# Kernel optimization log

Hardware: AMD Instinct MI355X
Metric: run time of the kernel (lower is better)

## Reference

```python
import jax, jax.numpy as jnp
import numpy as np


def setup_inputs() -> dict:
    key = jax.random.key(0)
    ks = jax.random.split(key, 8)
    B, C, H, W = 4, 256, 56, 56
    Cq = C // 8
    s = 0.05  # small init scale for conv weights, like kaiming-ish for 1x1 convs
    return {
        "x": jax.random.normal(ks[0], (B, C, H, W), jnp.float32),
        "Wq": jax.random.normal(ks[1], (Cq, C), jnp.float32) * s,
        "bq": jax.random.normal(ks[2], (Cq,), jnp.float32) * s,
        "Wk": jax.random.normal(ks[3], (Cq, C), jnp.float32) * s,
        "bk": jax.random.normal(ks[4], (Cq,), jnp.float32) * s,
        "Wv": jax.random.normal(ks[5], (C, C), jnp.float32) * s,
        "bv": jax.random.normal(ks[6], (C,), jnp.float32) * s,
        "gamma": jax.random.normal(ks[7], (1,), jnp.float32),
    }


def reference(x, Wq, bq, Wk, bk, Wv, bv, gamma):
    B, C, H, W = x.shape
    N = H * W
    xf = x.reshape(B, C, N)  # flatten spatial

    # 1x1 convs == channel matmuls
    q = jnp.einsum('oc,bcn->bon', Wq, xf) + bq[None, :, None]   # [B,Cq,N]
    k = jnp.einsum('oc,bcn->bon', Wk, xf) + bk[None, :, None]   # [B,Cq,N]
    v = jnp.einsum('oc,bcn->bon', Wv, xf) + bv[None, :, None]   # [B,C,N]

    # lipschitz_norm from weights: u=||Q||_F, v=max row-norm of K^T, w=max row-norm of V^T
    u = jnp.linalg.norm(Wq)
    vn = jnp.max(jnp.linalg.norm(Wk.T, axis=1))
    wn = jnp.max(jnp.linalg.norm(Wv.T, axis=1))
    norm_value = jnp.maximum(u * vn, u * wn)  # maximum(u*v, v*u, u*w)

    # energy[b,i,j] = <q[:,i], k[:,j]>, scaled by custom Lipschitz norm
    energy = jnp.einsum('bci,bcj->bij', q, k) / norm_value      # [B,N,N]
    attention = jax.nn.softmax(energy, axis=-1)

    # out[b,c,i] = sum_j v[b,c,j] * attention[b,i,j]
    out = jnp.einsum('bcj,bij->bci', v, attention).reshape(B, C, H, W)

    # lipschitz_bound: exp(sqrt(3)) * sqrt(N/C) + 2*sqrt(6)
    bound = np.float32(np.exp(np.sqrt(3.0)) * np.sqrt(N / C) + 2.0 * np.sqrt(6.0))
    out = out / bound

    return gamma * out + x
```

## Files before the change

kernel.cpp:

```cpp
#include <hip/hip_runtime.h>

#define N_SP 3136
#define C_CH 256
#define CQ   32
#define NB   4
#define JT   64
#define NJT  49
#define QT   64
#define INV_BOUND 0.04051569f
#define LOG2E 1.44269504f

typedef __attribute__((ext_vector_type(8))) short bf16x8;
typedef __attribute__((ext_vector_type(4))) float f32x4;
typedef __attribute__((ext_vector_type(2))) long long l64x2;
typedef unsigned short u16;
typedef unsigned int   u32;
typedef unsigned char  u8;
typedef long long      l64;

#define MFMA16(a,b,c) __builtin_amdgcn_mfma_f32_16x16x32_bf16(a,b,c,0,0,0)
#define MFMA8(a,b,c)  __builtin_amdgcn_mfma_f32_16x16x32_bf8_fp8(a,b,c,0,0,0)

__device__ __forceinline__ u16 f2b(float f) {
    u32 u = __builtin_bit_cast(u32, f);
    u += 0x7fffu + ((u >> 16) & 1u);
    return (u16)(u >> 16);
}
__device__ __forceinline__ u8 f2fp8(float f) {
    return (u8)(__builtin_amdgcn_cvt_pk_fp8_f32(f, f, 0, false) & 0xff);
}
__device__ __forceinline__ void dma16(const void* g, void* l) {
    __builtin_amdgcn_global_load_lds((const __attribute__((address_space(1))) u32*)g,
                                     (__attribute__((address_space(3))) u32*)l, 16, 0, 0);
}

__global__ __launch_bounds__(256) void stage1_kernel(
    const float* __restrict__ x, const float* __restrict__ Wq,
    const float* __restrict__ Wk, const float* __restrict__ Wv,
    u8* __restrict__ xT, u8* __restrict__ Wqb, u8* __restrict__ Wkb,
    u8* __restrict__ Wvb, float* __restrict__ scale_out,
    float* __restrict__ kmax)
{
    __shared__ float smem[64 * 65];
    const int t = threadIdx.x;
    const int bid = blockIdx.x;

    if (bid < 784) {
        float (*tile)[65] = (float(*)[65])smem;
        const int xcd = bid & 7, slot = bid >> 3;
        const int b = xcd >> 1;
        const int i = slot * 2 + (xcd & 1);
        const int ct = i & 3, nt = i >> 2;
        const int c0 = ct * 64, n0 = nt * 64;
        const int cc = t >> 4, nn4 = (t & 15) * 4;
        #pragma unroll
        for (int k = 0; k < 4; ++k) {
            int cl = cc + k * 16;
            float4 v = *(const float4*)(x + (size_t)(b * C_CH + c0 + cl) * N_SP + n0 + nn4);
            tile[cl][nn4] = v.x; tile[cl][nn4 + 1] = v.y;
            tile[cl][nn4 + 2] = v.z; tile[cl][nn4 + 3] = v.w;
        }
        __syncthreads();
        const int c4 = (t & 15) * 4, nn = t >> 4;
        #pragma unroll
        for (int k = 0; k < 4; ++k) {
            int nl = nn + k * 16;
            ushort4 o;
            o.x = f2b(tile[c4 + 0][nl]); o.y = f2b(tile[c4 + 1][nl]);
            o.z = f2b(tile[c4 + 2][nl]); o.w = f2b(tile[c4 + 3][nl]);
            const int off = ((c0 + c4) * 2) ^ ((nl & 15) << 5);
            *(ushort4*)(xT + (size_t)(b * N_SP + n0 + nl) * 512 + off) = o;
        }
    } else if (bid < 864) {
        int idx = (bid - 784) * 256 + t;
        const float* src; u8* dst; int off;
        if (idx < 2048)      { src = Wq; dst = Wqb; off = idx; }
        else if (idx < 4096) { src = Wk; dst = Wkb; off = idx - 2048; }
        else                 { src = Wv; dst = Wvb; off = idx - 4096; }
        float4 v = *(const float4*)(src + off * 4);
        ushort4 o; o.x = f2b(v.x); o.y = f2b(v.y); o.z = f2b(v.z); o.w = f2b(v.w);
        const int row = off >> 6, inner = (off & 63) * 8;
        *(ushort4*)(dst + row * 512 + (inner ^ ((row & 15) << 5))) = o;
    } else {
        if (t < NB) kmax[t] = 0.f;
        float* red = smem;
        float u2 = 0.f;
        for (int i = t; i < CQ * C_CH; i += 256) { float w = Wq[i]; u2 += w * w; }
        red[t] = u2; __syncthreads();
        #pragma unroll
        for (int s = 128; s > 0; s >>= 1) { if (t < s) red[t] += red[t + s]; __syncthreads(); }
        float u2t = red[0]; __syncthreads();
        float vn2 = 0.f;
        for (int o = 0; o < CQ; ++o)   { float w = Wk[o * C_CH + t]; vn2 += w * w; }
        float wn2 = 0.f;
        for (int o = 0; o < C_CH; ++o) { float w = Wv[o * C_CH + t]; wn2 += w * w; }
        red[t] = fmaxf(vn2, wn2); __syncthreads();
        #pragma unroll
        for (int s = 128; s > 0; s >>= 1) { if (t < s) red[t] = fmaxf(red[t], red[t + s]); __syncthreads(); }
        if (t == 0) scale_out[0] = 1.0f / (sqrtf(u2t) * sqrtf(red[0]));
    }
}

__global__ __launch_bounds__(256) void qkv_mfma(
    const u8* __restrict__ xT, const u8* __restrict__ Wqb,
    const u8* __restrict__ Wkb, const u8* __restrict__ Wvb,
    const float* __restrict__ bq, const float* __restrict__ bk,
    const float* __restrict__ bv, const float* __restrict__ scale_p,
    u16* __restrict__ qT, u8* __restrict__ Kg, u8* __restrict__ Vg,
    float* __restrict__ qnorm, float* __restrict__ kmax)
{
    __shared__ __align__(16) u8 xTl[32768];
    __shared__ __align__(16) u8 Wl[32768];

    const int t = threadIdx.x;
    const int xcd = blockIdx.x & 7, slot = blockIdx.x >> 3;
    const int b = xcd >> 1;
    const int i = slot * 2 + (xcd & 1);
    if (i >= 245) return;
    const int split = i / 49, nt = i % 49;
    const int w = t >> 6, lane = t & 63, li = t & 15, g = (t >> 4) & 3;
    const int n = nt * 64 + w * 16 + li;
    const int r0 = (split - 1) * 64;
    const f32x4 zero = {0.f, 0.f, 0.f, 0.f};

    {
        const u8* xsrc = xT + (size_t)(b * N_SP + nt * 64) * 512;
        #pragma unroll
        for (int k = 0; k < 8; ++k)
            dma16(xsrc + w * 8192 + k * 1024 + lane * 16, xTl + w * 8192 + k * 1024);
        if (split == 0) {
            #pragma unroll
            for (int k = 0; k < 4; ++k)
                dma16(Wqb + w * 4096 + k * 1024 + lane * 16, Wl + w * 4096 + k * 1024);
            #pragma unroll
            for (int k = 0; k < 4; ++k)
                dma16(Wkb + w * 4096 + k * 1024 + lane * 16, Wl + 16384 + w * 4096 + k * 1024);
        } else {
            const u8* wsrc = Wvb + (size_t)r0 * 512;
            #pragma unroll
            for (int k = 0; k < 8; ++k)
                dma16(wsrc + w * 8192 + k * 1024 + lane * 16, Wl + w * 8192 + k * 1024);
        }
    }
    asm volatile("s_waitcnt vmcnt(0)" ::: "memory");
    __syncthreads();

    const int swz = li << 5;
    bf16x8 xf[8];
    #pragma unroll
    for (int ks = 0; ks < 8; ++ks)
        xf[ks] = *(const bf16x8*)(xTl + (w * 16 + li) * 512 + ((ks * 64 + 16 * g) ^ swz));

    if (split == 0) {
        f32x4 aq0 = zero, aq1 = zero, ak0 = zero, ak1 = zero;
        #pragma unroll
        for (int ks = 0; ks < 8; ++ks) {
            const int o = (ks * 64 + 16 * g) ^ swz;
            bf16x8 w0 = *(const bf16x8*)(Wl + li * 512 + o);
            bf16x8 w1 = *(const bf16x8*)(Wl + (16 + li) * 512 + o);
            bf16x8 w2 = *(const bf16x8*)(Wl + 16384 + li * 512 + o);
            bf16x8 w3 = *(const bf16x8*)(Wl + 16384 + (16 + li) * 512 + o);
            aq0 = MFMA16(w0, xf[ks], aq0);
            aq1 = MFMA16(w1, xf[ks], aq1);
            ak0 = MFMA16(w2, xf[ks], ak0);
            ak1 = MFMA16(w3, xf[ks], ak1);
        }
        const float scf = scale_p[0] * LOG2E;
        f32x4 bq0 = *(const f32x4*)(bq + 4 * g);
        f32x4 bq1 = *(const f32x4*)(bq + 16 + 4 * g);
        f32x4 bk0 = *(const f32x4*)(bk + 4 * g);
        f32x4 bk1 = *(const f32x4*)(bk + 16 + 4 * g);
        float qn2 = 0.f, kn2 = 0.f;
        ushort4 s0, s1;
        #pragma unroll
        for (int r = 0; r < 4; ++r) {
            float q0 = (aq0[r] + bq0[r]) * scf;
            float q1 = (aq1[r] + bq1[r]) * scf;
            qn2 += q0 * q0 + q1 * q1;
            ((u16*)&s0)[r] = f2b(q0); ((u16*)&s1)[r] = f2b(q1);
        }
        *(ushort4*)(qT + (size_t)(b * N_SP + n) * CQ + 4 * g)      = s0;
        *(ushort4*)(qT + (size_t)(b * N_SP + n) * CQ + 16 + 4 * g) = s1;
        #pragma unroll
        for (int r = 0; r < 4; ++r) {
            float k0 = ak0[r] + bk0[r];
            float k1 = ak1[r] + bk1[r];
            kn2 += k0 * k0 + k1 * k1;
            ((u16*)&s0)[r] = f2b(k0); ((u16*)&s1)[r] = f2b(k1);
        }
        u8* krow = Kg + ((size_t)b * N_SP + n) * 64;
        const int swn = ((n >> 1) & 3) << 4;
        *(ushort4*)(krow + ((8 * g) ^ swn))      = s0;
        *(ushort4*)(krow + ((32 + 8 * g) ^ swn)) = s1;

        qn2 += __shfl_xor(qn2, 16); qn2 += __shfl_xor(qn2, 32);
        kn2 += __shfl_xor(kn2, 16); kn2 += __shfl_xor(kn2, 32);
        if (g == 0) qnorm[b * N_SP + n] = sqrtf(qn2);
        float kn = sqrtf(kn2);
        #pragma unroll
        for (int d = 1; d < 16; d <<= 1) kn = fmaxf(kn, __shfl_xor(kn, d));
        if ((t & 63) == 0) atomicMax((int*)(kmax + b), __float_as_int(kn));
    } else {
        f32x4 a[4] = {zero, zero, zero, zero};
        #pragma unroll
        for (int ks = 0; ks < 8; ++ks) {
            const int o = (ks * 64 + 16 * g) ^ swz;
            #pragma unroll
            for (int fr = 0; fr < 4; ++fr) {
                bf16x8 wf = *(const bf16x8*)(Wl + (fr * 16 + li) * 512 + o);
                a[fr] = MFMA16(wf, xf[ks], a[fr]);
            }
        }
        const int jj = w * 16 + li;
        const int p = ((jj >> 5) & 1) * 8 + ((jj >> 3) & 3) * 16 + (jj & 7);
        u8* vtile = Vg + (size_t)(b * NJT + nt) * 16384;
        #pragma unroll
        for (int fr = 0; fr < 4; ++fr) {
            f32x4 bb = *(const f32x4*)(bv + r0 + fr * 16 + 4 * g);
            #pragma unroll
            for (int r = 0; r < 4; ++r) {
                const int c = r0 + fr * 16 + 4 * g + r;
                vtile[c * 64 + (p ^ (((c >> 1) & 3) << 4))] = f2fp8(a[fr][r] + bb[r]);
            }
        }
    }
}

__global__ __launch_bounds__(512, 6) void attn_mfma(
    const u16* __restrict__ qT, const u8* __restrict__ Kg,
    const u8* __restrict__ Vg, const float* __restrict__ x,
    const float* __restrict__ gamma_p, const float* __restrict__ qnorm,
    const float* __restrict__ kmax, float* __restrict__ out)
{
    __shared__ __align__(16) u8 smem[40960];
    u8* const Vl = smem;
    u8* const Kl = smem + 24576;
    u8* const Pl = smem + 36864;

    const int t = threadIdx.x;
    const int w = t >> 6, li = t & 15, g = (t >> 4) & 3;
    const int jh = w & 3, qh = w >> 2;
    const int swz = ((li >> 1) & 3) << 4;

    const int bid = blockIdx.x;
    const int b = bid / 98, rem = bid % 98;
    const int qt = rem >> 1, h = rem & 1;
    const int i0 = qt * QT;

    const u16* qTb = qT + (size_t)b * N_SP * CQ;
    const u8*  Kbb = Kg + (size_t)b * N_SP * 64;
    const u8*  Vbb = Vg + (size_t)b * NJT * 16384 + h * 8192;
    const float kmb = kmax[b];
    const f32x4 zero = {0.f, 0.f, 0.f, 0.f};

    const int qA = 2 * qh, qB = 2 * qh + 1;
    const bf16x8 qfA = *(const bf16x8*)(qTb + (size_t)(i0 + qA * 16 + li) * CQ + 8 * g);
    const bf16x8 qfB = *(const bf16x8*)(qTb + (size_t)(i0 + qB * 16 + li) * CQ + 8 * g);
    const float mrA = qnorm[b * N_SP + i0 + qA * 16 + li] * kmb;
    const float mrB = qnorm[b * N_SP + i0 + qB * 16 + li] * kmb;

    f32x4 acc[4];
    #pragma unroll
    for (int qq = 0; qq < 4; ++qq) acc[qq] = zero;
    float lsA = 0.f, lsB = 0.f;

    #define ISSUE(jt_, s_) do {                                               \
        dma16(Vbb + (size_t)(jt_) * 16384 + t * 16,                           \
              Vl + (s_) * 8192 + w * 1024);                                   \
        if (t < 256)                                                          \
            dma16(Kbb + (size_t)(jt_) * 4096 + t * 16,                        \
                  Kl + (s_) * 4096 + w * 1024);                               \
    } while (0)

    ISSUE(0, 0);
    ISSUE(1, 1);

    const int p0 = ((jh >> 1) & 1) * 8 + ((jh * 2 + (g >> 1)) & 3) * 16 + 4 * (g & 1);

    int cur = 0;
    for (int it = 0; it < NJT; ++it) {
        if (w < 4) asm volatile("s_waitcnt vmcnt(2) lgkmcnt(0)" ::: "memory");
        else       asm volatile("s_waitcnt vmcnt(1) lgkmcnt(0)" ::: "memory");
        __builtin_amdgcn_s_barrier();
        asm volatile("" ::: "memory");

        {
            int jn = it + 2; if (jn > NJT - 1) jn = NJT - 1;
            int s2 = cur + 2; if (s2 >= 3) s2 -= 3;
            ISSUE(jn, s2);
        }

        const u8* Kc = Kl + cur * 4096;
        bf16x8 kf = *(const bf16x8*)(Kc + (jh * 16 + li) * 64 + ((16 * g) ^ swz));
        f32x4 sA = MFMA16(kf, qfA, zero);
        f32x4 sB = MFMA16(kf, qfB, zero);
        {
            float a0 = exp2f(sA[0] - mrA), a1 = exp2f(sA[1] - mrA);
            float a2 = exp2f(sA[2] - mrA), a3 = exp2f(sA[3] - mrA);
            lsA += (a0 + a1) + (a2 + a3);
            int pk = __builtin_amdgcn_cvt_pk_bf8_f32(a0, a1, 0, false);
            pk = __builtin_amdgcn_cvt_pk_bf8_f32(a2, a3, pk, true);
            *(u32*)(Pl + (qA * 16 + li) * 64 + (p0 ^ swz)) = (u32)pk;
            float b0 = exp2f(sB[0] - mrB), b1 = exp2f(sB[1] - mrB);
            float b2 = exp2f(sB[2] - mrB), b3 = exp2f(sB[3] - mrB);
            lsB += (b0 + b1) + (b2 + b3);
            pk = __builtin_amdgcn_cvt_pk_bf8_f32(b0, b1, 0, false);
            pk = __builtin_amdgcn_cvt_pk_bf8_f32(b2, b3, pk, true);
            *(u32*)(Pl + (qB * 16 + li) * 64 + (p0 ^ swz)) = (u32)pk;
        }
        asm volatile("s_waitcnt lgkmcnt(0)" ::: "memory");
        __builtin_amdgcn_s_barrier();
        asm volatile("" ::: "memory");

        const u8* Vc = Vl + cur * 8192;
        __builtin_amdgcn_s_setprio(1);
        l64x2 pa0 = *(const l64x2*)(Pl + (0 * 16 + li) * 64 + ((16 * g) ^ swz));
        l64x2 pa1 = *(const l64x2*)(Pl + (1 * 16 + li) * 64 + ((16 * g) ^ swz));
        l64x2 pa2 = *(const l64x2*)(Pl + (2 * 16 + li) * 64 + ((16 * g) ^ swz));
        l64x2 pa3 = *(const l64x2*)(Pl + (3 * 16 + li) * 64 + ((16 * g) ^ swz));
        l64x2 v0  = *(const l64x2*)(Vc + (w * 16 + li) * 64 + ((16 * g) ^ swz));
        acc[0] = MFMA8(pa0[0], v0[0], acc[0]);
        acc[1] = MFMA8(pa1[0], v0[0], acc[1]);
        acc[2] = MFMA8(pa2[0], v0[0], acc[2]);
        acc[3] = MFMA8(pa3[0], v0[0], acc[3]);
        acc[0] = MFMA8(pa0[1], v0[1], acc[0]);
        acc[1] = MFMA8(pa1[1], v0[1], acc[1]);
        acc[2] = MFMA8(pa2[1], v0[1], acc[2]);
        acc[3] = MFMA8(pa3[1], v0[1], acc[3]);
        __builtin_amdgcn_s_setprio(0);

        ++cur; if (cur == 3) cur = 0;
    }
    #undef ISSUE

    lsA += __shfl_xor(lsA, 16); lsA += __shfl_xor(lsA, 32);
    lsB += __shfl_xor(lsB, 16); lsB += __shfl_xor(lsB, 32);
    __syncthreads();
    float* red       = (float*)Pl;
    float* red_final = (float*)(Pl + 1024);
    if ((t & 63) < 16) {
        red[w * 32 + li]      = lsA;
        red[w * 32 + 16 + li] = lsB;
    }
    __syncthreads();
    if (t < 64) {
        const int hh = t >> 4, l2 = t & 15;
        float s = 0.f;
        #pragma unroll
        for (int jw = 0; jw < 4; ++jw)
            s += red[((hh >> 1) * 4 + jw) * 32 + (hh & 1) * 16 + l2];
        red_final[t] = s;
    }
    __syncthreads();

    const float gsc = gamma_p[0] * INV_BOUND;
    const int c = h * 128 + w * 16 + li;
    #pragma unroll
    for (int qq = 0; qq < 4; ++qq) {
        f32x4 lsv = *(const f32x4*)(red_final + qq * 16 + 4 * g);
        f32x4 rinv;
        #pragma unroll
        for (int r = 0; r < 4; ++r) rinv[r] = gsc / lsv[r];
        const size_t base = ((size_t)b * C_CH + c) * N_SP + i0 + qq * 16 + 4 * g;
        float4 xv = *(const float4*)(x + base);
        float4 o;
        o.x = acc[qq][0] * rinv[0] + xv.x;
        o.y = acc[qq][1] * rinv[1] + xv.y;
        o.z = acc[qq][2] * rinv[2] + xv.z;
        o.w = acc[qq][3] * rinv[3] + xv.w;
        *(float4*)(out + base) = o;
    }
}

extern "C" void kernel_launch(void* const* d_in, const int* in_sizes, int n_in,
                              void* d_out, int out_size, void* d_ws, size_t ws_size,
                              hipStream_t stream)
{
    const float* x  = (const float*)d_in[0];
    const float* Wq = (const float*)d_in[1];
    const float* bq = (const float*)d_in[2];
    const float* Wk = (const float*)d_in[3];
    const float* bk = (const float*)d_in[4];
    const float* Wv = (const float*)d_in[5];
    const float* bv = (const float*)d_in[6];
    const float* gm = (const float*)d_in[7];
    float* out = (float*)d_out;
    float* ws  = (float*)d_ws;

    float* scale = ws;
    float* kmax  = ws + 4;
    float* qnorm = ws + 8;
    u8* Wqb = (u8*)(ws + 8 + NB * N_SP);
    u8* Wkb = Wqb + 32 * 512;
    u8* Wvb = Wkb + 32 * 512;
    u8* xT  = Wvb + 256 * 512;
    u16* qT = (u16*)(xT + (size_t)NB * N_SP * 512);
    u8* Kg  = (u8*)(qT + (size_t)NB * N_SP * CQ);
    u8* Vg  = Kg + (size_t)NB * N_SP * 64;

    stage1_kernel<<<865, 256, 0, stream>>>(x, Wq, Wk, Wv, xT, Wqb, Wkb, Wvb, scale, kmax);
    qkv_mfma<<<984, 256, 0, stream>>>(xT, Wqb, Wkb, Wvb, bq, bk, bv, scale, qT, Kg, Vg, qnorm, kmax);
    attn_mfma<<<392, 512, 0, stream>>>(qT, Kg, Vg, x, gm, qnorm, kmax, out);
}
```

Before: 93.10 us.

## Merge channel halves into 1024-thread attention blocks with 4-stage pipeline

Each attention block now covers all 256 output channels with 16 waves, so the QK^T scores and softmax probabilities for a query tile are computed once per tile rather than duplicated across two channel-half blocks. Each wave now handles one 16-query slice instead of two, and the K/V prefetch ring grows from 3 to 4 stages with deeper wait counts. The trade-off is only 196 blocks, fewer than the device's compute units, plus about 84KB of LDS per block. That lowers occupancy and can leave CUs idle.

```diff
diff --git a/kernel.cpp b/kernel.cpp
--- a/kernel.cpp
+++ b/kernel.cpp
@@ -226,47 +226,43 @@
     }
 }
 
-__global__ __launch_bounds__(512, 6) void attn_mfma(
+__global__ __launch_bounds__(1024) void attn_mfma(
     const u16* __restrict__ qT, const u8* __restrict__ Kg,
     const u8* __restrict__ Vg, const float* __restrict__ x,
     const float* __restrict__ gamma_p, const float* __restrict__ qnorm,
     const float* __restrict__ kmax, float* __restrict__ out)
 {
-    __shared__ __align__(16) u8 smem[40960];
+    __shared__ __align__(16) u8 smem[86016];
     u8* const Vl = smem;
-    u8* const Kl = smem + 24576;
-    u8* const Pl = smem + 36864;
+    u8* const Kl = smem + 65536;
+    u8* const Pl = smem + 81920;
 
     const int t = threadIdx.x;
     const int w = t >> 6, li = t & 15, g = (t >> 4) & 3;
     const int jh = w & 3, qh = w >> 2;
     const int swz = ((li >> 1) & 3) << 4;
 
-    const int bid = blockIdx.x;
-    const int b = bid / 98, rem = bid % 98;
-    const int qt = rem >> 1, h = rem & 1;
+    const int b  = blockIdx.x / NJT;
+    const int qt = blockIdx.x % NJT;
     const int i0 = qt * QT;
 
     const u16* qTb = qT + (size_t)b * N_SP * CQ;
     const u8*  Kbb = Kg + (size_t)b * N_SP * 64;
-    const u8*  Vbb = Vg + (size_t)b * NJT * 16384 + h * 8192;
+    const u8*  Vbb = Vg + (size_t)b * NJT * 16384;
     const float kmb = kmax[b];
     const f32x4 zero = {0.f, 0.f, 0.f, 0.f};
 
-    const int qA = 2 * qh, qB = 2 * qh + 1;
-    const bf16x8 qfA = *(const bf16x8*)(qTb + (size_t)(i0 + qA * 16 + li) * CQ + 8 * g);
-    const bf16x8 qfB = *(const bf16x8*)(qTb + (size_t)(i0 + qB * 16 + li) * CQ + 8 * g);
-    const float mrA = qnorm[b * N_SP + i0 + qA * 16 + li] * kmb;
-    const float mrB = qnorm[b * N_SP + i0 + qB * 16 + li] * kmb;
+    const bf16x8 qf = *(const bf16x8*)(qTb + (size_t)(i0 + qh * 16 + li) * CQ + 8 * g);
+    const float  mr = qnorm[b * N_SP + i0 + qh * 16 + li] * kmb;
 
     f32x4 acc[4];
     #pragma unroll
     for (int qq = 0; qq < 4; ++qq) acc[qq] = zero;
-    float lsA = 0.f, lsB = 0.f;
+    float ls = 0.f;
 
     #define ISSUE(jt_, s_) do {                                               \
         dma16(Vbb + (size_t)(jt_) * 16384 + t * 16,                           \
-              Vl + (s_) * 8192 + w * 1024);                                   \
+              Vl + (s_) * 16384 + w * 1024);                                  \
         if (t < 256)                                                          \
             dma16(Kbb + (size_t)(jt_) * 4096 + t * 16,                        \
                   Kl + (s_) * 4096 + w * 1024);                               \
@@ -274,45 +270,38 @@
 
     ISSUE(0, 0);
     ISSUE(1, 1);
+    ISSUE(2, 2);
 
     const int p0 = ((jh >> 1) & 1) * 8 + ((jh * 2 + (g >> 1)) & 3) * 16 + 4 * (g & 1);
 
-    int cur = 0;
     for (int it = 0; it < NJT; ++it) {
-        if (w < 4) asm volatile("s_waitcnt vmcnt(2) lgkmcnt(0)" ::: "memory");
-        else       asm volatile("s_waitcnt vmcnt(1) lgkmcnt(0)" ::: "memory");
+        const int cur = it & 3;
+        if (w < 4) asm volatile("s_waitcnt vmcnt(4) lgkmcnt(0)" ::: "memory");
+        else       asm volatile("s_waitcnt vmcnt(2) lgkmcnt(0)" ::: "memory");
         __builtin_amdgcn_s_barrier();
         asm volatile("" ::: "memory");
 
         {
-            int jn = it + 2; if (jn > NJT - 1) jn = NJT - 1;
-            int s2 = cur + 2; if (s2 >= 3) s2 -= 3;
-            ISSUE(jn, s2);
+            int jn = it + 3; if (jn > NJT - 1) jn = NJT - 1;
+            ISSUE(jn, (cur + 3) & 3);
         }
 
         const u8* Kc = Kl + cur * 4096;
         bf16x8 kf = *(const bf16x8*)(Kc + (jh * 16 + li) * 64 + ((16 * g) ^ swz));
-        f32x4 sA = MFMA16(kf, qfA, zero);
-        f32x4 sB = MFMA16(kf, qfB, zero);
+        f32x4 s = MFMA16(kf, qf, zero);
         {
-            float a0 = exp2f(sA[0] - mrA), a1 = exp2f(sA[1] - mrA);
-            float a2 = exp2f(sA[2] - mrA), a3 = exp2f(sA[3] - mrA);
-            lsA += (a0 + a1) + (a2 + a3);
+            float a0 = exp2f(s[0] - mr), a1 = exp2f(s[1] - mr);
+            float a2 = exp2f(s[2] - mr), a3 = exp2f(s[3] - mr);
+            ls += (a0 + a1) + (a2 + a3);
             int pk = __builtin_amdgcn_cvt_pk_bf8_f32(a0, a1, 0, false);
             pk = __builtin_amdgcn_cvt_pk_bf8_f32(a2, a3, pk, true);
-            *(u32*)(Pl + (qA * 16 + li) * 64 + (p0 ^ swz)) = (u32)pk;
-            float b0 = exp2f(sB[0] - mrB), b1 = exp2f(sB[1] - mrB);
-            float b2 = exp2f(sB[2] - mrB), b3 = exp2f(sB[3] - mrB);
-            lsB += (b0 + b1) + (b2 + b3);
-            pk = __builtin_amdgcn_cvt_pk_bf8_f32(b0, b1, 0, false);
-            pk = __builtin_amdgcn_cvt_pk_bf8_f32(b2, b3, pk, true);
-            *(u32*)(Pl + (qB * 16 + li) * 64 + (p0 ^ swz)) = (u32)pk;
+            *(u32*)(Pl + (qh * 16 + li) * 64 + (p0 ^ swz)) = (u32)pk;
         }
         asm volatile("s_waitcnt lgkmcnt(0)" ::: "memory");
         __builtin_amdgcn_s_barrier();
         asm volatile("" ::: "memory");
 
-        const u8* Vc = Vl + cur * 8192;
+        const u8* Vc = Vl + cur * 16384;
         __builtin_amdgcn_s_setprio(1);
         l64x2 pa0 = *(const l64x2*)(Pl + (0 * 16 + li) * 64 + ((16 * g) ^ swz));
         l64x2 pa1 = *(const l64x2*)(Pl + (1 * 16 + li) * 64 + ((16 * g) ^ swz));
@@ -328,33 +317,25 @@
         acc[2] = MFMA8(pa2[1], v0[1], acc[2]);
         acc[3] = MFMA8(pa3[1], v0[1], acc[3]);
         __builtin_amdgcn_s_setprio(0);
-
-        ++cur; if (cur == 3) cur = 0;
     }
     #undef ISSUE
 
-    lsA += __shfl_xor(lsA, 16); lsA += __shfl_xor(lsA, 32);
-    lsB += __shfl_xor(lsB, 16); lsB += __shfl_xor(lsB, 32);
+    ls += __shfl_xor(ls, 16); ls += __shfl_xor(ls, 32);
     __syncthreads();
     float* red       = (float*)Pl;
     float* red_final = (float*)(Pl + 1024);
-    if ((t & 63) < 16) {
-        red[w * 32 + li]      = lsA;
-        red[w * 32 + 16 + li] = lsB;
-    }
+    if ((t & 63) < 16) red[w * 16 + li] = ls;
     __syncthreads();
     if (t < 64) {
-        const int hh = t >> 4, l2 = t & 15;
-        float s = 0.f;
-        #pragma unroll
-        for (int jw = 0; jw < 4; ++jw)
-            s += red[((hh >> 1) * 4 + jw) * 32 + (hh & 1) * 16 + l2];
+        const int qh2 = t >> 4, l2 = t & 15;
+        float s = red[(qh2 * 4 + 0) * 16 + l2] + red[(qh2 * 4 + 1) * 16 + l2]
+                + red[(qh2 * 4 + 2) * 16 + l2] + red[(qh2 * 4 + 3) * 16 + l2];
         red_final[t] = s;
     }
     __syncthreads();
 
     const float gsc = gamma_p[0] * INV_BOUND;
-    const int c = h * 128 + w * 16 + li;
+    const int c = w * 16 + li;
     #pragma unroll
     for (int qq = 0; qq < 4; ++qq) {
         f32x4 lsv = *(const f32x4*)(red_final + qq * 16 + 4 * g);
@@ -400,5 +381,5 @@
 
     stage1_kernel<<<865, 256, 0, stream>>>(x, Wq, Wk, Wv, xT, Wqb, Wkb, Wvb, scale, kmax);
     qkv_mfma<<<984, 256, 0, stream>>>(xT, Wqb, Wkb, Wvb, bq, bk, bv, scale, qT, Kg, Vg, qnorm, kmax);
-    attn_mfma<<<392, 512, 0, stream>>>(qT, Kg, Vg, x, gm, qnorm, kmax, out);
-}
+    attn_mfma<<<196, 1024, 0, stream>>>(qT, Kg, Vg, x, gm, qnorm, kmax, out);
+}
```

After: 85.57 us. 8.1% less time.
